# Performance work log

Measured on AMD Instinct MI355X. Metric: run time of the kernel, lower is better.

## Reference

```python
import jax, jax.numpy as jnp
import numpy as np

IMG = 512.0          # input H = W
SCORE_THR = 0.05
IOU_THR = 0.5
K_PRE = 1000         # pre-NMS candidates per image
MAX_DET = 300
CLS_OFF = 10000.0    # class-offset trick => per-class NMS


def _make_anchors():
    strides = [8, 16, 32, 64]
    sizes = [32.0, 64.0, 128.0, 256.0]
    ars = [0.5, 1.0, 2.0]
    out = []
    for s, sz in zip(strides, sizes):
        f = int(512 // s)
        ys, xs = np.meshgrid(np.arange(f), np.arange(f), indexing='ij')
        cx = (xs.reshape(-1) + 0.5) * s
        cy = (ys.reshape(-1) + 0.5) * s
        for ar in ars:
            w = sz * np.sqrt(ar)
            h = sz / np.sqrt(ar)
            out.append(np.stack([cx - w / 2, cy - h / 2, cx + w / 2, cy + h / 2], axis=1))
    return np.concatenate(out, axis=0).astype(np.float32)  # (16320, 4)


def setup_inputs() -> dict:
    key = jax.random.key(0)
    k1, k2 = jax.random.split(key)
    anchors = jnp.asarray(_make_anchors())
    B, C = 16, 80
    A = anchors.shape[0]
    cls_preds = jax.random.normal(k1, (B, A, C), jnp.float32) - 2.0  # logits, sigmoid ~0.12
    box_preds = jax.random.normal(k2, (B, A, 4), jnp.float32) * 0.2  # box deltas
    return {"cls_preds": cls_preds, "box_preds": box_preds, "anchors": anchors}


def _decode(anchors, deltas):
    aw = anchors[:, 2] - anchors[:, 0]
    ah = anchors[:, 3] - anchors[:, 1]
    acx = anchors[:, 0] + 0.5 * aw
    acy = anchors[:, 1] + 0.5 * ah
    cx = deltas[:, 0] * aw + acx
    cy = deltas[:, 1] * ah + acy
    w = jnp.exp(deltas[:, 2]) * aw
    h = jnp.exp(deltas[:, 3]) * ah
    b = jnp.stack([cx - 0.5 * w, cy - 0.5 * h, cx + 0.5 * w, cy + 0.5 * h], axis=1)
    return jnp.clip(b, 0.0, IMG)  # clamp to image, H == W == IMG


def _iou_matrix(b):
    area = jnp.maximum(b[:, 2] - b[:, 0], 0.0) * jnp.maximum(b[:, 3] - b[:, 1], 0.0)
    lt = jnp.maximum(b[:, None, :2], b[None, :, :2])
    rb = jnp.minimum(b[:, None, 2:], b[None, :, 2:])
    wh = jnp.clip(rb - lt, 0.0)
    inter = wh[..., 0] * wh[..., 1]
    return inter / jnp.maximum(area[:, None] + area[None, :] - inter, 1e-6)


def _per_image(cls_p, box_p, anchors):
    scores = jax.nn.sigmoid(cls_p)                 # (A, C)
    boxes = _decode(anchors, box_p)                # (A, 4)
    ms = scores.max(axis=1)                        # best class score
    lb = jnp.argmax(scores, axis=1)                # best class id (0-indexed)
    s = jnp.where(ms > SCORE_THR, ms, -1.0)        # score-threshold filter
    top_s, idx = jax.lax.top_k(s, K_PRE)           # pre-NMS candidates, sorted desc
    b = boxes[idx]
    l = lb[idx]
    ob = b + l[:, None].astype(b.dtype) * CLS_OFF  # per-class NMS via offset
    iou = _iou_matrix(ob)                          # (K_PRE, K_PRE)
    rng = jnp.arange(K_PRE)

    def body(i, keep):
        sup = (iou[i] > IOU_THR) & keep[i] & (rng > i)
        return keep & ~sup

    keep = jax.lax.fori_loop(0, K_PRE, body, top_s > 0.0)  # greedy NMS
    fs_all = jnp.where(keep, top_s, -1.0)
    fs, fi = jax.lax.top_k(fs_all, MAX_DET)
    ok = fs > 0.0
    out_boxes = jnp.where(ok[:, None], b[fi], 0.0)
    out_scores = jnp.where(ok, fs, 0.0)
    out_labels = jnp.where(ok, l[fi] + 1, 0)  # labels are 1-indexed
    return out_boxes, out_scores, out_labels


def reference(cls_preds, box_preds, anchors):
    return jax.vmap(lambda c, bp: _per_image(c, bp, anchors))(cls_preds, box_preds)
```

## Files before the change

kernel.cpp:

```cpp
#include <hip/hip_runtime.h>
#include <cstdint>
#include <cmath>

#define NB 16
#define AANCH 16320
#define NCLS 80
#define KPRE 1000
#define MAXDET 300
#define NCH 16
#define CCAP 4096
#define HBINS 8192

#define THR_LOGIT -2.9444389791664403f

__global__ __launch_bounds__(256) void k_score(const float* __restrict__ cls,
                                               uint32_t* __restrict__ key,
                                               int* __restrict__ label) {
    int b = blockIdx.y;
    int a0 = blockIdx.x * 64;
    int t = threadIdx.x;
    int al = t >> 2, g = t & 3;
    const float4* p = (const float4*)(cls + ((size_t)b * AANCH + a0) * NCLS) + al * 20 + g;
    float best = -3e38f; int bi = 0;
#pragma unroll
    for (int i = 0; i < 5; ++i) {
        float4 v = p[4 * i];
        int c0 = 4 * g + 16 * i;
        if (v.x > best) { best = v.x; bi = c0 + 0; }
        if (v.y > best) { best = v.y; bi = c0 + 1; }
        if (v.z > best) { best = v.z; bi = c0 + 2; }
        if (v.w > best) { best = v.w; bi = c0 + 3; }
    }
#pragma unroll
    for (int m = 1; m <= 2; m <<= 1) {
        float ob = __shfl_xor(best, m, 64);
        int oi = __shfl_xor(bi, m, 64);
        if (ob > best || (ob == best && oi < bi)) { best = ob; bi = oi; }
    }
    if (g == 0) {
        uint32_t k = 0;
        if (best > THR_LOGIT) {
            uint32_t ub = __float_as_uint(best);
            k = (ub & 0x80000000u) ? ~ub : (ub | 0x80000000u);
        }
        int ag = a0 + al;
        key[(size_t)b * AANCH + ag] = k;
        label[(size_t)b * AANCH + ag] = bi;
    }
}

__global__ __launch_bounds__(1024, 1) void k_frd(const uint32_t* __restrict__ key,
                                                 const int* __restrict__ label,
                                                 const float* __restrict__ boxp,
                                                 const float* __restrict__ anchors,
                                                 float4* __restrict__ topBox,
                                                 float* __restrict__ topScore,
                                                 int* __restrict__ topLabel,
                                                 uint32_t* __restrict__ validCnt) {
    __shared__ uint32_t kk[AANCH];
    __shared__ unsigned long long candbuf[CCAP];
    __shared__ uint32_t part[256];
    __shared__ uint32_t s_pivot, s_pos;
    uint32_t* hist = (uint32_t*)candbuf;
    unsigned long long* cand = candbuf;
    int b = blockIdx.x, tid = threadIdx.x;
    for (int i = tid; i < HBINS; i += 1024) hist[i] = 0;
    if (tid == 0) s_pos = 0;
    __syncthreads();
    const uint32_t* kb = key + (size_t)b * AANCH;
    for (int i = tid; i < AANCH; i += 1024) {
        uint32_t k = kb[i];
        kk[i] = k;
        atomicAdd(&hist[k >> 19], 1u);
    }
    __syncthreads();
    if (tid < 256) {
        uint32_t s = 0;
#pragma unroll
        for (int i = 0; i < 32; ++i) s += hist[tid * 32 + ((i + tid) & 31)];
        part[tid] = s;
    }
    __syncthreads();
    if (tid == 0) {
        uint32_t acc = 0; int tc = 0;
        for (int t2 = 255; t2 >= 0; --t2) {
            if (acc + part[t2] >= (uint32_t)KPRE) { tc = t2; break; }
            acc += part[t2];
        }
        uint32_t p1 = 0;
        for (int bin = tc * 32 + 31; bin >= tc * 32; --bin) {
            if (acc + hist[bin] >= (uint32_t)KPRE) { p1 = (uint32_t)bin; break; }
            acc += hist[bin];
        }
        s_pivot = p1;
        uint32_t nvalid = (uint32_t)AANCH - hist[0];
        validCnt[b] = nvalid < (uint32_t)KPRE ? nvalid : (uint32_t)KPRE;
    }
    __syncthreads();
    uint32_t piv = s_pivot;
    for (int i = tid; i < AANCH; i += 1024) {
        uint32_t k = kk[i];
        if ((k >> 19) >= piv) {
            uint32_t pos = atomicAdd(&s_pos, 1u);
            if (pos < CCAP)
                cand[pos] = ((unsigned long long)k << 32) | (uint32_t)(~i);
        }
    }
    __syncthreads();
    int C = (int)(s_pos < CCAP ? s_pos : CCAP);
    for (int c = tid; c < C; c += 1024) {
        unsigned long long mine = cand[c];
        uint32_t r = 0;
#pragma unroll 4
        for (int j = 0; j < C; ++j) r += (cand[j] > mine);
        if (r >= (uint32_t)KPRE) continue;
        uint32_t mk = (uint32_t)(mine >> 32);
        uint32_t idx = ~(uint32_t)mine;
        const float* an = anchors + (size_t)idx * 4;
        float a0 = an[0], a1 = an[1], a2 = an[2], a3 = an[3];
        const float* dp = boxp + ((size_t)b * AANCH + idx) * 4;
        float d0 = dp[0], d1 = dp[1], d2 = dp[2], d3 = dp[3];
        float aw = a2 - a0, ah = a3 - a1;
        float acx = a0 + 0.5f * aw, acy = a1 + 0.5f * ah;
        float cx = d0 * aw + acx, cy = d1 * ah + acy;
        float w = expf(d2) * aw, hh = expf(d3) * ah;
        float x1 = fminf(fmaxf(cx - 0.5f * w, 0.0f), 512.0f);
        float y1 = fminf(fmaxf(cy - 0.5f * hh, 0.0f), 512.0f);
        float x2 = fminf(fmaxf(cx + 0.5f * w, 0.0f), 512.0f);
        float y2 = fminf(fmaxf(cy + 0.5f * hh, 0.0f), 512.0f);
        float score;
        if (mk == 0u) {
            score = -1.0f;
        } else {
            uint32_t ub = (mk & 0x80000000u) ? (mk ^ 0x80000000u) : ~mk;
            score = 1.0f / (1.0f + expf(-__uint_as_float(ub)));
        }
        int t = b * KPRE + (int)r;
        topBox[t] = make_float4(x1, y1, x2, y2);
        topScore[t] = score;
        topLabel[t] = label[(size_t)b * AANCH + idx];
    }
}

__global__ __launch_bounds__(64) void k_maskT(const float4* __restrict__ topBox,
                                              const int* __restrict__ topLabel,
                                              unsigned long long* __restrict__ maskT) {
    int b = blockIdx.y;
    int tt = blockIdx.x;
    int rb = 0;
    while (tt >= NCH - rb) { tt -= NCH - rb; ++rb; }
    int cb = rb + tt;
    __shared__ float4 cob[64];
    __shared__ float car[64];
    int lane = threadIdx.x;
    int j = cb * 64 + lane;
    float4 vj;
    if (j < KPRE) {
        vj = topBox[b * KPRE + j];
        float off = (float)topLabel[b * KPRE + j] * 10000.0f;
        vj.x += off; vj.y += off; vj.z += off; vj.w += off;
    } else {
        vj = make_float4(-3e37f, -3e37f, -3e37f, -3e37f);
    }
    cob[lane] = vj;
    car[lane] = fmaxf(vj.z - vj.x, 0.0f) * fmaxf(vj.w - vj.y, 0.0f);
    int i = rb * 64 + lane;
    float4 bi;
    if (i < KPRE) {
        bi = topBox[b * KPRE + i];
        float off = (float)topLabel[b * KPRE + i] * 10000.0f;
        bi.x += off; bi.y += off; bi.z += off; bi.w += off;
    } else {
        bi = make_float4(-3e37f, -3e37f, -3e37f, -3e37f);
    }
    float ai = fmaxf(bi.z - bi.x, 0.0f) * fmaxf(bi.w - bi.y, 0.0f);
    __syncthreads();
    unsigned long long myword = 0;
#pragma unroll 8
    for (int jj = 0; jj < 64; ++jj) {
        int jg = cb * 64 + jj;
        float4 bj = cob[jj];
        float ltx = fmaxf(bi.x, bj.x), lty = fmaxf(bi.y, bj.y);
        float rbx = fminf(bi.z, bj.z), rby = fminf(bi.w, bj.w);
        float wx = fmaxf(rbx - ltx, 0.0f), wy = fmaxf(rby - lty, 0.0f);
        float inter = wx * wy;
        float iou = inter / fmaxf(ai + car[jj] - inter, 1e-6f);
        bool pred = (iou > 0.5f) && (i < jg) && (i < KPRE) && (jg < KPRE);
        unsigned long long bal = __ballot(pred);
        if (lane == jj) myword = bal;
    }
    maskT[(((size_t)b * NCH + rb) * NCH + cb) * 64 + lane] = myword;
}

__global__ __launch_bounds__(64) void k_nmsout(const unsigned long long* __restrict__ maskT,
                                               const uint32_t* __restrict__ validCnt,
                                               const float4* __restrict__ topBox,
                                               const float* __restrict__ topScore,
                                               const int* __restrict__ topLabel,
                                               float* __restrict__ out) {
    int b = blockIdx.x, lane = threadIdx.x;
    int V = (int)validCnt[b];
    const unsigned long long* mtb = maskT + (size_t)b * NCH * NCH * 64;
    unsigned long long km[NCH];
#pragma unroll
    for (int s = 0; s < NCH; ++s) km[s] = 0ull;
    int count = 0;
    unsigned long long mt[NCH];
#pragma unroll
    for (int s = 0; s < NCH; ++s) mt[s] = mtb[((size_t)s * NCH + 0) * 64 + lane];
#pragma unroll
    for (int c = 0; c < NCH; ++c) {
        bool go = (c * 64 < V) && (count < MAXDET);
        unsigned long long cur[NCH];
#pragma unroll
        for (int s = 0; s < NCH; ++s) cur[s] = mt[s];
        if (go && c + 1 < NCH) {
#pragma unroll
            for (int s = 0; s < NCH; ++s) mt[s] = mtb[((size_t)s * NCH + (c + 1)) * 64 + lane];
        }
        unsigned long long kmask = 0;
        if (go) {
            unsigned long long dd = 0;
            unsigned long long colbits = cur[c];
#pragma unroll
            for (int s = 0; s < NCH; ++s) dd |= (cur[s] & km[s]);
            bool dead = dd != 0ull;
            bool valid = (c * 64 + lane) < V;
            bool kept = false;
            while (count < MAXDET) {
                unsigned long long undec = __ballot((!dead) && (!kept) && valid);
                if (undec == 0ull) break;
                int f = __builtin_ctzll(undec);
                kmask |= 1ull << f;
                ++count;
                if (lane == f) kept = true;
                dead = dead || (((colbits >> f) & 1ull) != 0ull);
            }
        }
        km[c] = kmask;
    }
    int pf[NCH + 1];
    pf[0] = 0;
#pragma unroll
    for (int cc = 0; cc < NCH; ++cc) pf[cc + 1] = pf[cc] + __popcll(km[cc]);
    int total = pf[NCH];
#pragma unroll
    for (int cc = 0; cc < NCH; ++cc) {
        unsigned long long m = km[cc];
        if ((m >> lane) & 1ull) {
            int slot = pf[cc] + __popcll(m & ((1ull << lane) - 1ull));
            int g = cc * 64 + lane;
            int tdx = b * MAXDET + slot;
            float4 box = topBox[b * KPRE + g];
            out[(size_t)tdx * 4 + 0] = box.x;
            out[(size_t)tdx * 4 + 1] = box.y;
            out[(size_t)tdx * 4 + 2] = box.z;
            out[(size_t)tdx * 4 + 3] = box.w;
            out[(size_t)NB * MAXDET * 4 + tdx] = topScore[b * KPRE + g];
            out[(size_t)NB * MAXDET * 5 + tdx] = (float)(topLabel[b * KPRE + g] + 1);
        }
    }
    for (int k2 = lane; k2 < MAXDET; k2 += 64) {
        if (k2 >= total) {
            int tdx = b * MAXDET + k2;
            out[(size_t)tdx * 4 + 0] = 0.0f;
            out[(size_t)tdx * 4 + 1] = 0.0f;
            out[(size_t)tdx * 4 + 2] = 0.0f;
            out[(size_t)tdx * 4 + 3] = 0.0f;
            out[(size_t)NB * MAXDET * 4 + tdx] = 0.0f;
            out[(size_t)NB * MAXDET * 5 + tdx] = 0.0f;
        }
    }
}

extern "C" void kernel_launch(void* const* d_in, const int* in_sizes, int n_in,
                              void* d_out, int out_size, void* d_ws, size_t ws_size,
                              hipStream_t stream) {
    const float* cls = (const float*)d_in[0];
    const float* boxp = (const float*)d_in[1];
    const float* anchors = (const float*)d_in[2];
    float* out = (float*)d_out;

    char* wsp = (char*)d_ws;
    size_t off = 0;
    auto carve = [&](size_t bytes) -> void* {
        void* p = wsp + off;
        off += (bytes + 255) & ~(size_t)255;
        return p;
    };
    unsigned long long* maskT = (unsigned long long*)carve((size_t)NB * NCH * NCH * 64 * 8);
    uint32_t* key       = (uint32_t*)carve((size_t)NB * AANCH * 4);
    int*      label     = (int*)carve((size_t)NB * AANCH * 4);
    float4*   topBox    = (float4*)carve((size_t)NB * KPRE * 16);
    float*    topScore  = (float*)carve((size_t)NB * KPRE * 4);
    int*      topLabel  = (int*)carve((size_t)NB * KPRE * 4);
    uint32_t* validCnt  = (uint32_t*)carve((size_t)NB * 4);
    (void)ws_size; (void)out_size; (void)n_in; (void)in_sizes;

    k_score<<<dim3(AANCH / 64, NB), 256, 0, stream>>>(cls, key, label);
    k_frd<<<NB, 1024, 0, stream>>>(key, label, boxp, anchors, topBox, topScore, topLabel,
                                   validCnt);
    k_maskT<<<dim3(136, NB), 64, 0, stream>>>(topBox, topLabel, maskT);
    k_nmsout<<<NB, 64, 0, stream>>>(maskT, validCnt, topBox, topScore, topLabel, out);
}
```

Measured before the change: 226.9 us.

## Split top-K select into filter and multi-block rank-and-decode kernels

The per-image single-block kernel that built candidates and ranked them with an O(C^2) count is split in two. A selection kernel writes the candidate list to global memory. A new kernel then spreads the rank counting and box decode over up to 8 blocks per image, with each thread ranking two candidates against shared-memory tiles. This gives the quadratic rank step more parallelism than the 16 blocks it had before, at the cost of an extra launch and a global round trip for the candidates.

```diff
diff --git a/kernel.cpp b/kernel.cpp
--- a/kernel.cpp
+++ b/kernel.cpp
@@ -49,20 +49,14 @@
     }
 }
 
-__global__ __launch_bounds__(1024, 1) void k_frd(const uint32_t* __restrict__ key,
-                                                 const int* __restrict__ label,
-                                                 const float* __restrict__ boxp,
-                                                 const float* __restrict__ anchors,
-                                                 float4* __restrict__ topBox,
-                                                 float* __restrict__ topScore,
-                                                 int* __restrict__ topLabel,
-                                                 uint32_t* __restrict__ validCnt) {
+__global__ __launch_bounds__(1024, 1) void k_fsel(const uint32_t* __restrict__ key,
+                                                  uint32_t* __restrict__ validCnt,
+                                                  uint32_t* __restrict__ candCount,
+                                                  unsigned long long* __restrict__ cand) {
     __shared__ uint32_t kk[AANCH];
-    __shared__ unsigned long long candbuf[CCAP];
+    __shared__ uint32_t hist[HBINS];
     __shared__ uint32_t part[256];
     __shared__ uint32_t s_pivot, s_pos;
-    uint32_t* hist = (uint32_t*)candbuf;
-    unsigned long long* cand = candbuf;
     int b = blockIdx.x, tid = threadIdx.x;
     for (int i = tid; i < HBINS; i += 1024) hist[i] = 0;
     if (tid == 0) s_pos = 0;
@@ -103,17 +97,50 @@
         if ((k >> 19) >= piv) {
             uint32_t pos = atomicAdd(&s_pos, 1u);
             if (pos < CCAP)
-                cand[pos] = ((unsigned long long)k << 32) | (uint32_t)(~i);
-        }
-    }
-    __syncthreads();
-    int C = (int)(s_pos < CCAP ? s_pos : CCAP);
-    for (int c = tid; c < C; c += 1024) {
-        unsigned long long mine = cand[c];
-        uint32_t r = 0;
+                cand[(size_t)b * CCAP + pos] = ((unsigned long long)k << 32) | (uint32_t)(~i);
+        }
+    }
+    __syncthreads();
+    if (tid == 0) candCount[b] = s_pos < CCAP ? s_pos : CCAP;
+}
+
+__global__ __launch_bounds__(256) void k_rankdec(const unsigned long long* __restrict__ cand,
+                                                 const uint32_t* __restrict__ candCount,
+                                                 const int* __restrict__ label,
+                                                 const float* __restrict__ boxp,
+                                                 const float* __restrict__ anchors,
+                                                 float4* __restrict__ topBox,
+                                                 float* __restrict__ topScore,
+                                                 int* __restrict__ topLabel) {
+    __shared__ unsigned long long tp[2048];
+    int b = blockIdx.y, tid = threadIdx.x;
+    int C = (int)candCount[b];
+    int base = blockIdx.x * 512;
+    if (base >= C) return;
+    const unsigned long long* cb = cand + (size_t)b * CCAP;
+    int c0 = base + tid, c1 = base + 256 + tid;
+    bool h0 = c0 < C, h1 = c1 < C;
+    unsigned long long m0 = h0 ? cb[c0] : 0ull;
+    unsigned long long m1 = h1 ? cb[c1] : 0ull;
+    uint32_t r0 = 0, r1 = 0;
+    for (int t0 = 0; t0 < C; t0 += 2048) {
+        int n = C - t0; if (n > 2048) n = 2048;
+        __syncthreads();
+        for (int j = tid; j < n; j += 256) tp[j] = cb[t0 + j];
+        __syncthreads();
 #pragma unroll 4
-        for (int j = 0; j < C; ++j) r += (cand[j] > mine);
-        if (r >= (uint32_t)KPRE) continue;
+        for (int j = 0; j < n; ++j) {
+            unsigned long long v = tp[j];
+            r0 += (v > m0);
+            r1 += (v > m1);
+        }
+    }
+#pragma unroll
+    for (int q = 0; q < 2; ++q) {
+        bool h = q == 0 ? h0 : h1;
+        uint32_t r = q == 0 ? r0 : r1;
+        unsigned long long mine = q == 0 ? m0 : m1;
+        if (!h || r >= (uint32_t)KPRE) continue;
         uint32_t mk = (uint32_t)(mine >> 32);
         uint32_t idx = ~(uint32_t)mine;
         const float* an = anchors + (size_t)idx * 4;
@@ -291,15 +318,18 @@
     unsigned long long* maskT = (unsigned long long*)carve((size_t)NB * NCH * NCH * 64 * 8);
     uint32_t* key       = (uint32_t*)carve((size_t)NB * AANCH * 4);
     int*      label     = (int*)carve((size_t)NB * AANCH * 4);
+    unsigned long long* cand = (unsigned long long*)carve((size_t)NB * CCAP * 8);
     float4*   topBox    = (float4*)carve((size_t)NB * KPRE * 16);
     float*    topScore  = (float*)carve((size_t)NB * KPRE * 4);
     int*      topLabel  = (int*)carve((size_t)NB * KPRE * 4);
     uint32_t* validCnt  = (uint32_t*)carve((size_t)NB * 4);
+    uint32_t* candCount = (uint32_t*)carve((size_t)NB * 4);
     (void)ws_size; (void)out_size; (void)n_in; (void)in_sizes;
 
     k_score<<<dim3(AANCH / 64, NB), 256, 0, stream>>>(cls, key, label);
-    k_frd<<<NB, 1024, 0, stream>>>(key, label, boxp, anchors, topBox, topScore, topLabel,
-                                   validCnt);
+    k_fsel<<<NB, 1024, 0, stream>>>(key, validCnt, candCount, cand);
+    k_rankdec<<<dim3(CCAP / 512, NB), 256, 0, stream>>>(cand, candCount, label, boxp, anchors,
+                                                        topBox, topScore, topLabel);
     k_maskT<<<dim3(136, NB), 64, 0, stream>>>(topBox, topLabel, maskT);
     k_nmsout<<<NB, 64, 0, stream>>>(maskT, validCnt, topBox, topScore, topLabel, out);
 }
```

Measured after the change: 217.1 us (median of 2 runs). 1.05x faster.
